# Kernel optimization log

Hardware: AMD Instinct MI355X
Metric: run time of the kernel (lower is better)

## Reference

```python
import jax, jax.numpy as jnp
import numpy as np

HID = 4096; H = 128; P = 64; N = 128; G = 8; K = 4; CH = 128
INTER = H * P                      # 8192
CONV_DIM = INTER + 2 * G * N       # 10240
PROJ = INTER + CONV_DIM + H        # 18560
EPS = 1e-5


def segsum(x):
    # stable segment-sum: out[..., i, j] = sum_{j < k <= i} x[..., k]; -inf above diagonal
    T = x.shape[-1]
    xe = jnp.repeat(x[..., None], T, axis=-1)          # [..., i, j] = x[..., i]
    strict = jnp.tril(jnp.ones((T, T), bool), -1)
    s = jnp.cumsum(jnp.where(strict, xe, 0.0), axis=-2)
    keep = jnp.tril(jnp.ones((T, T), bool), 0)
    return jnp.where(keep, s, -jnp.inf)


def setup_inputs() -> dict:
    key = jax.random.key(0)
    ks = jax.random.split(key, 6)
    b, L = 2, 2048
    hidden_states = jax.random.normal(ks[0], (b, L, HID), jnp.float32)
    in_proj_w = jax.random.normal(ks[1], (PROJ, HID), jnp.float32) * (HID ** -0.5)
    conv_w = jax.random.normal(ks[2], (CONV_DIM, 1, K), jnp.float32) * 0.2
    conv_b = jax.random.normal(ks[3], (CONV_DIM,), jnp.float32) * 0.02
    dt_bias = jnp.ones((H,), jnp.float32)
    A_log = jnp.log(jnp.arange(1, H + 1, dtype=jnp.float32))
    D = jnp.ones((H,), jnp.float32)
    norm_weight = jnp.ones((INTER,), jnp.float32)
    out_proj_w = jax.random.normal(ks[4], (HID, INTER), jnp.float32) * (INTER ** -0.5)
    return dict(hidden_states=hidden_states, in_proj_w=in_proj_w, conv_w=conv_w, conv_b=conv_b,
                dt_bias=dt_bias, A_log=A_log, D=D, norm_weight=norm_weight, out_proj_w=out_proj_w)


def _mamba2(hidden_states, in_proj_w, conv_w, conv_b, dt_bias, A_log, D, norm_weight, out_proj_w):
    b, L, _ = hidden_states.shape
    nchunk = L // CH  # seq_len chosen to be a multiple of chunk_size (pad_size = 0)

    # in_proj and split into gate | conv path (x,B,C) | dt
    proj = hidden_states @ in_proj_w.T
    gate, hBC, dt = jnp.split(proj, [INTER, INTER + CONV_DIM], axis=-1)

    # causal depthwise conv1d (padding k-1, truncate) + SiLU
    xp = jnp.pad(hBC.transpose(0, 2, 1), ((0, 0), (0, 0), (K - 1, 0)))
    xc = jax.lax.conv_general_dilated(xp, conv_w, (1,), 'VALID',
                                      feature_group_count=CONV_DIM,
                                      dimension_numbers=('NCW', 'OIW', 'NCW'))
    hBC = jax.nn.silu((xc + conv_b[None, :, None]).transpose(0, 2, 1))
    hs, Bx, Cx = jnp.split(hBC, [INTER, INTER + G * N], axis=-1)

    A = -jnp.exp(A_log)                      # [H]
    dt = jax.nn.softplus(dt + dt_bias)       # time_step_limit = (0, inf) -> clamp is no-op

    hs = hs.reshape(b, L, H, P)
    rep = H // G
    Bm = jnp.tile(Bx.reshape(b, L, G, N), (1, 1, rep, 1))   # matches torch .repeat
    Cm = jnp.tile(Cx.reshape(b, L, G, N), (1, 1, rep, 1))

    D_res = D[None, None, :, None] * hs      # [b,L,H,P]

    # discretize and chunk
    X = (hs * dt[..., None]).reshape(b, nchunk, CH, H, P)
    A_dt = (A[None, None, :] * dt).reshape(b, nchunk, CH, H).transpose(0, 3, 1, 2)  # [b,H,c,l]
    Bc = Bm.reshape(b, nchunk, CH, H, N)
    Cc = Cm.reshape(b, nchunk, CH, H, N)
    A_cs = jnp.cumsum(A_dt, axis=-1)

    # 1. intra-chunk (diagonal blocks)
    Lmat = jnp.exp(segsum(A_dt))                              # [b,H,c,l,s]
    Gm = jnp.einsum('bclhn,bcshn->bclsh', Cc, Bc)
    M = Gm * Lmat.transpose(0, 2, 3, 4, 1)                    # [b,c,l,s,H]
    Y_diag = jnp.einsum('bclsh,bcshp->bclhp', M, X)

    # 2. per-chunk states
    decay_states = jnp.exp(A_cs[..., -1:] - A_cs)             # [b,H,c,l]
    B_decay = Bc * decay_states.transpose(0, 2, 3, 1)[..., None]
    states = jnp.einsum('bclhn,bclhp->bchpn', B_decay, X)     # [b,c,H,P,N]

    # 3. inter-chunk recurrence
    states = jnp.concatenate([jnp.zeros_like(states[:, :1]), states], axis=1)
    A_last = jnp.pad(A_cs[..., -1], ((0, 0), (0, 0), (1, 0)))  # [b,H,c+1]
    decay_chunk = jnp.exp(segsum(A_last)).transpose(0, 3, 2, 1)  # [b,c+1,c+1,H]
    new_states = jnp.einsum('bzjh,bzhpn->bjhpn', decay_chunk, states)
    prev_states = new_states[:, :-1]                           # [b,c,H,P,N]

    # 4. state -> output
    sdo = jnp.exp(A_cs).transpose(0, 2, 3, 1)                  # [b,c,l,H]
    Y_off = jnp.einsum('bclhn,bchpn->bclhp', Cc, prev_states) * sdo[..., None]

    y = (Y_diag + Y_off).reshape(b, L, H, P) + D_res
    scan_out = y.reshape(b, L, INTER)

    # gated group RMSNorm (norm_before_gate=False: gate first, then group-RMS)
    xg = scan_out * jax.nn.silu(gate)
    xr = xg.reshape(b, L, G, INTER // G)
    xr = xr * jax.lax.rsqrt(jnp.mean(xr * xr, axis=-1, keepdims=True) + EPS)
    normed = xr.reshape(b, L, INTER) * norm_weight

    return normed @ out_proj_w.T


def reference(hidden_states, in_proj_w, conv_w, conv_b, dt_bias, A_log, D, norm_weight, out_proj_w):
    return _mamba2(hidden_states, in_proj_w, conv_w, conv_b, dt_bias, A_log, D, norm_weight, out_proj_w)
```

## Files before the change

kernel.cpp:

```cpp
#include <hip/hip_runtime.h>

#define NH 128
#define PD 64
#define NSD 128
#define NG 8
#define CHK 128
#define HIDD 4096
#define INTER_D 8192
#define CONV_D 10240
#define PROJ_D 18560
#define SEQ 2048
#define ROWS 4096
#define NCH 16

typedef __attribute__((ext_vector_type(8))) short bf16x8;
typedef __attribute__((ext_vector_type(4))) float f32x4;

__device__ __forceinline__ unsigned short f2bf(float f) {
  unsigned int u = __float_as_uint(f);
  u += 0x7FFF + ((u >> 16) & 1);
  return (unsigned short)(u >> 16);
}
__device__ __forceinline__ float bf2f(unsigned short s) {
  return __uint_as_float(((unsigned int)s) << 16);
}

__device__ __forceinline__ void gld16(const unsigned short* g, unsigned short* l) {
  __builtin_amdgcn_global_load_lds(
      (__attribute__((address_space(1))) const void*)g,
      (__attribute__((address_space(3))) void*)l, 16, 0, 0);
}

#define BAR() __builtin_amdgcn_s_barrier()
#define SCHED() __builtin_amdgcn_sched_barrier(0)
#define VMCNT(n) asm volatile("s_waitcnt vmcnt(" #n ")" ::: "memory")

__device__ __forceinline__ bf16x8 ldsfrag(const unsigned short* slot, int row, int kslot) {
  int byte = row * 128 + (((kslot ^ (row & 7)) << 4));
  return *(const bf16x8*)((const char*)slot + byte);
}

__global__ __launch_bounds__(256) void cvt_kernel(const float* __restrict__ in,
                                                  unsigned short* __restrict__ out,
                                                  size_t n) {
  size_t i = ((size_t)blockIdx.x * 256 + threadIdx.x) * 4;
  if (i < n) {
    float4 f = *(const float4*)(in + i);
    ushort4 o;
    o.x = f2bf(f.x); o.y = f2bf(f.y); o.z = f2bf(f.z); o.w = f2bf(f.w);
    *(ushort4*)(out + i) = o;
  }
}

template <int OUT_BF16>
__global__ __launch_bounds__(512, 2) void gemm256(const unsigned short* __restrict__ A,
                                                  const unsigned short* __restrict__ B,
                                                  unsigned short* __restrict__ outb,
                                                  float* __restrict__ outf,
                                                  int Nreal, int Ks, int Kl, int koff) {
  __shared__ unsigned short lds[8][8192];
  int tid = threadIdx.x, l = tid & 63, w = tid >> 6;
  int wm = w >> 2, wn = w & 3;
  int il = l & 15, fog = l >> 4;
  int bid = blockIdx.x;
  int xcd = bid & 7, local = bid >> 3;
  int mt = xcd * 2 + (local & 1), nt = local >> 1;
  const unsigned short* Abase = A + (size_t)mt * 256 * Ks + koff;
  const unsigned short* Bbase = B + (size_t)nt * 256 * Ks + koff;
  int NT = Kl >> 6;

  f32x4 acc[2][2][4][2];
#pragma unroll
  for (int a = 0; a < 2; ++a)
#pragma unroll
    for (int b = 0; b < 2; ++b)
#pragma unroll
      for (int m = 0; m < 4; ++m)
#pragma unroll
        for (int n = 0; n < 2; ++n) acc[a][b][m][n] = (f32x4){0.f, 0.f, 0.f, 0.f};

  auto STG = [&](int tt, int ty) {
    int tc = tt < NT ? tt : NT - 1;
    const unsigned short* g = ((ty & 1) ? Bbase : Abase) + (size_t)((ty >> 1) * 128) * Ks + tc * 64;
    unsigned short* sp = (unsigned short*)lds[(tt & 1) * 4 + ty];
#pragma unroll
    for (int j = 0; j < 2; ++j) {
      int row = (j * 8 + w) * 8 + (l >> 3);
      int scol = ((l & 7) ^ (row & 7)) * 8;
      gld16(g + (size_t)row * Ks + scol, sp + (j * 8 + w) * 512);
    }
  };

#define LDA(SLOT)                                          \
  _Pragma("unroll") for (int mi = 0; mi < 4; ++mi)         \
  _Pragma("unroll") for (int kk = 0; kk < 2; ++kk)         \
      av[mi][kk] = ldsfrag(SLOT, wm * 64 + mi * 16 + il, kk * 4 + fog);
#define LDB(QN, SLOT)                                      \
  _Pragma("unroll") for (int ni = 0; ni < 2; ++ni)         \
  _Pragma("unroll") for (int kk = 0; kk < 2; ++kk)         \
      bv[QN][ni][kk] = ldsfrag(SLOT, wn * 32 + ni * 16 + il, kk * 4 + fog);
#define MFMA_PH(QM, QN)                                    \
  _Pragma("unroll") for (int mi = 0; mi < 4; ++mi)         \
  _Pragma("unroll") for (int ni = 0; ni < 2; ++ni)         \
  _Pragma("unroll") for (int kk = 0; kk < 2; ++kk)         \
      acc[QM][QN][mi][ni] = __builtin_amdgcn_mfma_f32_16x16x32_bf16( \
          av[mi][kk], bv[QN][ni][kk], acc[QM][QN][mi][ni], 0, 0, 0);

  STG(0, 0); STG(0, 1); STG(0, 3); STG(0, 2);
  VMCNT(2);
  BAR(); SCHED();

  for (int t = 0; t < NT; ++t) {
    const unsigned short* sA0 = lds[(t & 1) * 4 + 0];
    const unsigned short* sB0 = lds[(t & 1) * 4 + 1];
    const unsigned short* sA1 = lds[(t & 1) * 4 + 2];
    const unsigned short* sB1 = lds[(t & 1) * 4 + 3];
    bf16x8 av[4][2], bv[2][2][2];
    LDA(sA0); LDB(0, sB0); LDB(1, sB1);
    STG(t + 1, 0); STG(t + 1, 1);
    BAR();
    __builtin_amdgcn_s_setprio(1);
    MFMA_PH(0, 0);
    __builtin_amdgcn_s_setprio(0);
    VMCNT(4);
    BAR(); SCHED();
    STG(t + 1, 3);
    __builtin_amdgcn_s_setprio(1);
    MFMA_PH(0, 1);
    __builtin_amdgcn_s_setprio(0);
    BAR();
    LDA(sA1);
    STG(t + 1, 2);
    BAR();
    __builtin_amdgcn_s_setprio(1);
    MFMA_PH(1, 0);
    __builtin_amdgcn_s_setprio(0);
    BAR();
    __builtin_amdgcn_s_setprio(1);
    MFMA_PH(1, 1);
    __builtin_amdgcn_s_setprio(0);
    VMCNT(2);
    BAR(); SCHED();
  }
  VMCNT(0);

  int rl = (l >> 4) * 4;
#pragma unroll
  for (int qm = 0; qm < 2; ++qm)
#pragma unroll
    for (int qn = 0; qn < 2; ++qn)
#pragma unroll
      for (int mi = 0; mi < 4; ++mi)
#pragma unroll
        for (int ni = 0; ni < 2; ++ni) {
          int grow = mt * 256 + qm * 128 + wm * 64 + mi * 16 + rl;
          int gcol = nt * 256 + qn * 128 + wn * 32 + ni * 16 + il;
          if (!OUT_BF16 || gcol < Nreal) {
#pragma unroll
            for (int r = 0; r < 4; ++r) {
              float v = acc[qm][qn][mi][ni][r];
              if (OUT_BF16)
                outb[(size_t)(grow + r) * Nreal + gcol] = f2bf(v);
              else
                outf[(size_t)(grow + r) * Nreal + gcol] = v;
            }
          }
        }
#undef LDA
#undef LDB
#undef MFMA_PH
}

__global__ __launch_bounds__(128) void dts_kernel(const unsigned short* __restrict__ proj,
                                                  const float* __restrict__ dt_bias,
                                                  const float* __restrict__ A_log,
                                                  float* __restrict__ dtg,
                                                  float* __restrict__ acsg) {
  int bc = blockIdx.x;
  int h = threadIdx.x;
  int b = bc >> 4, c = bc & 15;
  float A = -__expf(A_log[h]);
  float bias = dt_bias[h];
  float cum = 0.f;
  int row0 = b * SEQ + c * CHK;
#pragma unroll 4
  for (int ll = 0; ll < CHK; ++ll) {
    float x = bf2f(proj[(size_t)(row0 + ll) * PROJ_D + (PROJ_D - NH) + h]) + bias;
    float d = (x > 20.f) ? x : log1pf(expf(x));
    dtg[(size_t)(row0 + ll) * NH + h] = d;
    cum += A * d;
    acsg[(((size_t)bc * NH) + h) * CHK + ll] = cum;
  }
}

__global__ __launch_bounds__(256) void conv_kernel(const unsigned short* __restrict__ proj,
                                                   const float* __restrict__ cw,
                                                   const float* __restrict__ cb,
                                                   unsigned short* __restrict__ xbc) {
  int ch0 = (blockIdx.x * 256 + threadIdx.x) * 8;
  int row = blockIdx.y;
  int b = row >> 11, ll = row & 2047;
  float4 cwv[8];
#pragma unroll
  for (int e = 0; e < 8; ++e) cwv[e] = *(const float4*)(cw + (ch0 + e) * 4);
  float acc[8];
#pragma unroll
  for (int e = 0; e < 8; ++e) acc[e] = cb[ch0 + e];
#pragma unroll
  for (int k = 0; k < 4; ++k) {
    int l2 = ll - 3 + k;
    if (l2 >= 0) {
      bf16x8 v = *(const bf16x8*)(proj + (size_t)(b * SEQ + l2) * PROJ_D + INTER_D + ch0);
#pragma unroll
      for (int e = 0; e < 8; ++e)
        acc[e] += bf2f(((unsigned short*)&v)[e]) * ((const float*)&cwv[e])[k];
    }
  }
  unsigned short o[8];
#pragma unroll
  for (int e = 0; e < 8; ++e) {
    float s = acc[e] / (1.f + __expf(-acc[e]));
    o[e] = f2bf(s);
  }
  *(int4*)(xbc + (size_t)row * CONV_D + ch0) = *(int4*)o;
}

__global__ __launch_bounds__(256) void e1b_kernel(const unsigned short* __restrict__ xbc,
                                                  const float* __restrict__ dtg,
                                                  const float* __restrict__ acsg,
                                                  unsigned short* __restrict__ states16) {
  int bid = blockIdx.x;
  int h = bid & 127, c = (bid >> 7) & 15, b = bid >> 11;
  int g = h & 7;
  int row0 = b * SEQ + c * CHK;
  __shared__ __align__(16) char smem[52736];
  unsigned short* XT = (unsigned short*)smem;
  unsigned short* BdT = (unsigned short*)(smem + 17408);
  float* Acs = (float*)(smem + 52224);
  int tid = threadIdx.x, lane = tid & 63, wv = tid >> 6;
  int fo = (lane >> 4) * 8, il = lane & 15, rl = (lane >> 4) * 4;
  if (tid < 128) Acs[tid] = acsg[(((size_t)(b * NCH + c) * NH) + h) * CHK + tid];
  __syncthreads();
#pragma unroll
  for (int j = 0; j < 4; ++j) {
    int q = tid + j * 256;
    int ll = q >> 3, p0 = (q & 7) * 8;
    int row = row0 + ll;
    float dtv = dtg[(size_t)row * NH + h];
    int4 raw = *(const int4*)(xbc + (size_t)row * CONV_D + h * PD + p0);
    unsigned short* u = (unsigned short*)&raw;
#pragma unroll
    for (int e = 0; e < 8; ++e) XT[(p0 + e) * 136 + ll] = f2bf(bf2f(u[e]) * dtv);
  }
#pragma unroll
  for (int j = 0; j < 8; ++j) {
    int q = tid + j * 256;
    int ll = q >> 4, n0 = (q & 15) * 8;
    float dec = __expf(Acs[CHK - 1] - Acs[ll]);
    int4 raw = *(const int4*)(xbc + (size_t)(row0 + ll) * CONV_D + INTER_D + g * NSD + n0);
    unsigned short* u = (unsigned short*)&raw;
#pragma unroll
    for (int e = 0; e < 8; ++e) BdT[(n0 + e) * 136 + ll] = f2bf(bf2f(u[e]) * dec);
  }
  __syncthreads();
  f32x4 st[8];
#pragma unroll
  for (int i = 0; i < 8; ++i) st[i] = (f32x4){0.f, 0.f, 0.f, 0.f};
#pragma unroll
  for (int ks = 0; ks < 4; ++ks) {
    bf16x8 a = *(const bf16x8*)&XT[(wv * 16 + il) * 136 + ks * 32 + fo];
#pragma unroll
    for (int ni = 0; ni < 8; ++ni) {
      bf16x8 bb = *(const bf16x8*)&BdT[(ni * 16 + il) * 136 + ks * 32 + fo];
      st[ni] = __builtin_amdgcn_mfma_f32_16x16x32_bf16(a, bb, st[ni], 0, 0, 0);
    }
  }
  size_t base = ((size_t)(b * NH + h) * NCH + c) * (PD * NSD);
#pragma unroll
  for (int ni = 0; ni < 8; ++ni) {
    int n = ni * 16 + il;
#pragma unroll
    for (int r = 0; r < 4; ++r) {
      int p = wv * 16 + rl + r;
      states16[base + p * NSD + n] = f2bf(st[ni][r]);
    }
  }
}

__global__ __launch_bounds__(256) void e2_kernel(const float* __restrict__ acsg,
                                                 const unsigned short* __restrict__ states16,
                                                 unsigned short* __restrict__ prevs) {
  int bid = blockIdx.x;
  int bh = bid >> 2, pg = bid & 3;
  int b = bh >> 7;
  int t = threadIdx.x;
  float S[8];
#pragma unroll
  for (int j = 0; j < 8; ++j) S[j] = 0.f;
  for (int c = 0; c < NCH; ++c) {
    float alast = acsg[(((size_t)((b * NCH + c) * NH) + (bh & 127))) * CHK + (CHK - 1)];
    float dec = __expf(alast);
    size_t base = ((size_t)bh * NCH + c) * (PD * NSD) + (size_t)pg * 2048 + (size_t)t * 8;
    bf16x8 v = *(const bf16x8*)(states16 + base);
    unsigned short o[8];
#pragma unroll
    for (int j = 0; j < 8; ++j) {
      o[j] = f2bf(S[j]);
      S[j] = S[j] * dec + bf2f(((unsigned short*)&v)[j]);
    }
    *(bf16x8*)(prevs + base) = *(bf16x8*)o;
  }
}

__global__ __launch_bounds__(512) void e13_kernel(const unsigned short* __restrict__ xbc,
                                                  const float* __restrict__ dtg,
                                                  const float* __restrict__ acsg,
                                                  const unsigned short* __restrict__ prevs,
                                                  const float* __restrict__ Dp,
                                                  unsigned short* __restrict__ ybh) {
  int bid = blockIdx.x;
  int h = bid & 127, c = (bid >> 7) & 15, b = bid >> 11;
  int g = h & 7;
  int row0 = b * SEQ + c * CHK;
  __shared__ __align__(16) char smem[70144];
  unsigned short* Cst = (unsigned short*)smem;
  unsigned short* Bst = (unsigned short*)(smem + 10240);
  unsigned short* Mt = (unsigned short*)smem;
  unsigned short* XT = (unsigned short*)(smem + 34816);
  unsigned short* Sp = (unsigned short*)(smem + 52224);
  float* Acs = (float*)(smem + 69632);
  int tid = threadIdx.x, lane = tid & 63, wv = tid >> 6;
  int fo = (lane >> 4) * 8, il = lane & 15, rl = (lane >> 4) * 4;
  if (tid < 128) Acs[tid] = acsg[(((size_t)(b * NCH + c) * NH) + h) * CHK + tid];

  f32x4 gm[8];
#pragma unroll
  for (int i = 0; i < 8; ++i) gm[i] = (f32x4){0.f, 0.f, 0.f, 0.f};
  bf16x8 cf[4];
  int srow = tid >> 2, scol = (tid & 3) * 8;
#pragma unroll
  for (int kc = 0; kc < 4; ++kc) {
    __syncthreads();
    *(int4*)(Cst + srow * 40 + scol) =
        *(const int4*)(xbc + (size_t)(row0 + srow) * CONV_D + INTER_D + NG * NSD + g * NSD + kc * 32 + scol);
    *(int4*)(Bst + srow * 40 + scol) =
        *(const int4*)(xbc + (size_t)(row0 + srow) * CONV_D + INTER_D + g * NSD + kc * 32 + scol);
    __syncthreads();
    bf16x8 a = *(const bf16x8*)&Cst[(wv * 16 + il) * 40 + fo];
    cf[kc] = a;
#pragma unroll
    for (int ni = 0; ni < 8; ++ni) {
      bf16x8 bb = *(const bf16x8*)&Bst[(ni * 16 + il) * 40 + fo];
      gm[ni] = __builtin_amdgcn_mfma_f32_16x16x32_bf16(a, bb, gm[ni], 0, 0, 0);
    }
  }
  __syncthreads();
#pragma unroll
  for (int ni = 0; ni < 8; ++ni) {
    int s = ni * 16 + il;
#pragma unroll
    for (int r = 0; r < 4; ++r) {
      int ll = wv * 16 + rl + r;
      float v = (s <= ll) ? gm[ni][r] * __expf(Acs[ll] - Acs[s]) : 0.f;
      Mt[ll * 136 + s] = f2bf(v);
    }
  }
#pragma unroll
  for (int j = 0; j < 2; ++j) {
    int q = tid + j * 512;
    int ll = q >> 3, p0 = (q & 7) * 8;
    int row = row0 + ll;
    float dtv = dtg[(size_t)row * NH + h];
    int4 raw = *(const int4*)(xbc + (size_t)row * CONV_D + h * PD + p0);
    unsigned short* u = (unsigned short*)&raw;
#pragma unroll
    for (int e = 0; e < 8; ++e) XT[(p0 + e) * 136 + ll] = f2bf(bf2f(u[e]) * dtv);
  }
  size_t sbase = ((size_t)(b * NH + h) * NCH + c) * (PD * NSD);
#pragma unroll
  for (int j = 0; j < 2; ++j) {
    int q = tid + j * 512;
    int p = q >> 4, n0 = (q & 15) * 8;
    *(int4*)(Sp + p * 136 + n0) = *(const int4*)(prevs + sbase + p * NSD + n0);
  }
  __syncthreads();
  f32x4 yd[4], yo[4];
#pragma unroll
  for (int i = 0; i < 4; ++i) {
    yd[i] = (f32x4){0.f, 0.f, 0.f, 0.f};
    yo[i] = (f32x4){0.f, 0.f, 0.f, 0.f};
  }
#pragma unroll
  for (int ks = 0; ks < 4; ++ks) {
    bf16x8 a = *(const bf16x8*)&Mt[(wv * 16 + il) * 136 + ks * 32 + fo];
#pragma unroll
    for (int pi = 0; pi < 4; ++pi) {
      bf16x8 bb = *(const bf16x8*)&XT[(pi * 16 + il) * 136 + ks * 32 + fo];
      bf16x8 sb = *(const bf16x8*)&Sp[(pi * 16 + il) * 136 + ks * 32 + fo];
      yd[pi] = __builtin_amdgcn_mfma_f32_16x16x32_bf16(a, bb, yd[pi], 0, 0, 0);
      yo[pi] = __builtin_amdgcn_mfma_f32_16x16x32_bf16(cf[ks], sb, yo[pi], 0, 0, 0);
    }
  }
  float dv = Dp[h];
#pragma unroll
  for (int pi = 0; pi < 4; ++pi) {
    int p = pi * 16 + il;
#pragma unroll
    for (int r = 0; r < 4; ++r) {
      int ll = wv * 16 + rl + r;
      int row = row0 + ll;
      float hsv = bf2f(xbc[(size_t)row * CONV_D + h * PD + p]);
      ybh[(size_t)row * INTER_D + h * PD + p] =
          f2bf(yd[pi][r] + yo[pi][r] * __expf(Acs[ll]) + dv * hsv);
    }
  }
}

__global__ __launch_bounds__(256) void fnorm_kernel(const unsigned short* __restrict__ ybh,
                                                    const unsigned short* __restrict__ proj,
                                                    const float* __restrict__ nw,
                                                    unsigned short* __restrict__ normed) {
  int row = blockIdx.x >> 3;
  int gg = blockIdx.x & 7;
  int t = threadIdx.x;
  int ch = gg * 1024 + t * 4;
  ushort4 yv = *(const ushort4*)(ybh + (size_t)row * INTER_D + ch);
  ushort4 gv = *(const ushort4*)(proj + (size_t)row * PROJ_D + ch);
  float v[4];
  float ss = 0.f;
  {
    const unsigned short* yp = (const unsigned short*)&yv;
    const unsigned short* gp = (const unsigned short*)&gv;
#pragma unroll
    for (int j = 0; j < 4; ++j) {
      float val = bf2f(yp[j]);
      float gt = bf2f(gp[j]);
      val *= gt / (1.f + __expf(-gt));
      v[j] = val;
      ss += val * val;
    }
  }
#pragma unroll
  for (int o = 1; o < 64; o <<= 1) ss += __shfl_xor(ss, o, 64);
  __shared__ float sred[4];
  if ((t & 63) == 0) sred[t >> 6] = ss;
  __syncthreads();
  float tot = sred[0] + sred[1] + sred[2] + sred[3];
  float rms = rsqrtf(tot / 1024.f + 1e-5f);
  float4 nwv = *(const float4*)(nw + ch);
  unsigned short o4[4];
  const float* nwp = (const float*)&nwv;
#pragma unroll
  for (int j = 0; j < 4; ++j) o4[j] = f2bf(v[j] * rms * nwp[j]);
  *(ushort4*)(normed + (size_t)row * INTER_D + ch) = *(ushort4*)o4;
}

extern "C" void kernel_launch(void* const* d_in, const int* in_sizes, int n_in,
                              void* d_out, int out_size, void* d_ws, size_t ws_size,
                              hipStream_t stream) {
  (void)in_sizes; (void)n_in; (void)out_size; (void)ws_size;
  const float* hs = (const float*)d_in[0];
  const float* w1 = (const float*)d_in[1];
  const float* cw = (const float*)d_in[2];
  const float* cb = (const float*)d_in[3];
  const float* dtb = (const float*)d_in[4];
  const float* alog = (const float*)d_in[5];
  const float* Dp = (const float*)d_in[6];
  const float* nw = (const float*)d_in[7];
  const float* w2 = (const float*)d_in[8];
  float* out = (float*)d_out;
  char* ws = (char*)d_ws;

  unsigned short* hsb = (unsigned short*)(ws);
  unsigned short* w1b = (unsigned short*)(ws + 33554432);
  unsigned short* w2b = (unsigned short*)(ws + 186646528);
  unsigned short* proj = (unsigned short*)(ws + 253755392);
  unsigned short* xbc = (unsigned short*)(ws + 405798912);
  float* dtg = (float*)(ws + 489684992);
  float* acsg = (float*)(ws + 491782144);
  unsigned short* states16 = (unsigned short*)(ws + 493879296);
  unsigned short* prevs = (unsigned short*)(ws + 560988160);
  unsigned short* ybh = (unsigned short*)(ws + 628097024);
  unsigned short* normed = (unsigned short*)(ws);

  cvt_kernel<<<dim3(16384), dim3(256), 0, stream>>>(hs, hsb, (size_t)ROWS * HIDD);
  cvt_kernel<<<dim3(74240), dim3(256), 0, stream>>>(w1, w1b, (size_t)PROJ_D * HIDD);
  cvt_kernel<<<dim3(32768), dim3(256), 0, stream>>>(w2, w2b, (size_t)HIDD * INTER_D);

  gemm256<1><<<dim3(16 * 73), dim3(512), 0, stream>>>(hsb, w1b, proj, nullptr,
                                                      PROJ_D, HIDD, HIDD, 0);
  dts_kernel<<<dim3(32), dim3(128), 0, stream>>>(proj, dtb, alog, dtg, acsg);
  conv_kernel<<<dim3(5, 4096), dim3(256), 0, stream>>>(proj, cw, cb, xbc);
  e1b_kernel<<<dim3(4096), dim3(256), 0, stream>>>(xbc, dtg, acsg, states16);
  e2_kernel<<<dim3(1024), dim3(256), 0, stream>>>(acsg, states16, prevs);
  e13_kernel<<<dim3(4096), dim3(512), 0, stream>>>(xbc, dtg, acsg, prevs, Dp, ybh);
  fnorm_kernel<<<dim3(32768), dim3(256), 0, stream>>>(ybh, proj, nw, normed);
  gemm256<0><<<dim3(16 * 16), dim3(512), 0, stream>>>(normed, w2b, nullptr, out,
                                                      HIDD, INTER_D, INTER_D, 0);
}
```

Measured before the change: 1.376 ms.

## Merge conversion launches, split dt scan into parallel pass, widen norm

New measurement: 1.313 ms. 1.05x faster.

```diff
diff --git a/kernel.cpp b/kernel.cpp
--- a/kernel.cpp
+++ b/kernel.cpp
@@ -40,16 +40,28 @@
   return *(const bf16x8*)((const char*)slot + byte);
 }
 
-__global__ __launch_bounds__(256) void cvt_kernel(const float* __restrict__ in,
-                                                  unsigned short* __restrict__ out,
-                                                  size_t n) {
-  size_t i = ((size_t)blockIdx.x * 256 + threadIdx.x) * 4;
-  if (i < n) {
-    float4 f = *(const float4*)(in + i);
-    ushort4 o;
-    o.x = f2bf(f.x); o.y = f2bf(f.y); o.z = f2bf(f.z); o.w = f2bf(f.w);
-    *(ushort4*)(out + i) = o;
-  }
+__global__ __launch_bounds__(256) void cvt_all_kernel(const float* __restrict__ hs,
+                                                      const float* __restrict__ w1,
+                                                      const float* __restrict__ w2,
+                                                      unsigned short* __restrict__ hsb,
+                                                      unsigned short* __restrict__ w1b,
+                                                      unsigned short* __restrict__ w2b) {
+  int bid = blockIdx.x;
+  const float* in;
+  unsigned short* out;
+  size_t base;
+  if (bid < 16384) {
+    in = hs; out = hsb; base = (size_t)bid * 1024;
+  } else if (bid < 16384 + 74240) {
+    in = w1; out = w1b; base = (size_t)(bid - 16384) * 1024;
+  } else {
+    in = w2; out = w2b; base = (size_t)(bid - 16384 - 74240) * 1024;
+  }
+  size_t i = base + (size_t)threadIdx.x * 4;
+  float4 f = *(const float4*)(in + i);
+  ushort4 o;
+  o.x = f2bf(f.x); o.y = f2bf(f.y); o.z = f2bf(f.z); o.w = f2bf(f.w);
+  *(ushort4*)(out + i) = o;
 }
 
 template <int OUT_BF16>
@@ -171,24 +183,28 @@
 #undef MFMA_PH
 }
 
-__global__ __launch_bounds__(128) void dts_kernel(const unsigned short* __restrict__ proj,
-                                                  const float* __restrict__ dt_bias,
-                                                  const float* __restrict__ A_log,
-                                                  float* __restrict__ dtg,
-                                                  float* __restrict__ acsg) {
+__global__ __launch_bounds__(256) void dtsa_kernel(const unsigned short* __restrict__ proj,
+                                                   const float* __restrict__ dt_bias,
+                                                   float* __restrict__ dtg) {
+  int idx = blockIdx.x * 256 + threadIdx.x;
+  int row = idx >> 7, h = idx & 127;
+  float x = bf2f(proj[(size_t)row * PROJ_D + (PROJ_D - NH) + h]) + dt_bias[h];
+  float d = (x > 20.f) ? x : log1pf(expf(x));
+  dtg[(size_t)row * NH + h] = d;
+}
+
+__global__ __launch_bounds__(128) void dtsb_kernel(const float* __restrict__ dtg,
+                                                   const float* __restrict__ A_log,
+                                                   float* __restrict__ acsg) {
   int bc = blockIdx.x;
   int h = threadIdx.x;
   int b = bc >> 4, c = bc & 15;
   float A = -__expf(A_log[h]);
-  float bias = dt_bias[h];
   float cum = 0.f;
   int row0 = b * SEQ + c * CHK;
-#pragma unroll 4
+#pragma unroll 8
   for (int ll = 0; ll < CHK; ++ll) {
-    float x = bf2f(proj[(size_t)(row0 + ll) * PROJ_D + (PROJ_D - NH) + h]) + bias;
-    float d = (x > 20.f) ? x : log1pf(expf(x));
-    dtg[(size_t)(row0 + ll) * NH + h] = d;
-    cum += A * d;
+    cum += A * dtg[(size_t)(row0 + ll) * NH + h];
     acsg[(((size_t)bc * NH) + h) * CHK + ll] = cum;
   }
 }
@@ -420,39 +436,43 @@
                                                     const unsigned short* __restrict__ proj,
                                                     const float* __restrict__ nw,
                                                     unsigned short* __restrict__ normed) {
-  int row = blockIdx.x >> 3;
-  int gg = blockIdx.x & 7;
-  int t = threadIdx.x;
-  int ch = gg * 1024 + t * 4;
-  ushort4 yv = *(const ushort4*)(ybh + (size_t)row * INTER_D + ch);
-  ushort4 gv = *(const ushort4*)(proj + (size_t)row * PROJ_D + ch);
-  float v[4];
+  int gid = blockIdx.x * 4 + (threadIdx.x >> 6);
+  int lane = threadIdx.x & 63;
+  int row = gid >> 3, gg = gid & 7;
+  int ch = gg * 1024 + lane * 16;
+  bf16x8 y0 = *(const bf16x8*)(ybh + (size_t)row * INTER_D + ch);
+  bf16x8 y1 = *(const bf16x8*)(ybh + (size_t)row * INTER_D + ch + 8);
+  bf16x8 g0 = *(const bf16x8*)(proj + (size_t)row * PROJ_D + ch);
+  bf16x8 g1 = *(const bf16x8*)(proj + (size_t)row * PROJ_D + ch + 8);
+  float v[16];
   float ss = 0.f;
-  {
-    const unsigned short* yp = (const unsigned short*)&yv;
-    const unsigned short* gp = (const unsigned short*)&gv;
-#pragma unroll
-    for (int j = 0; j < 4; ++j) {
-      float val = bf2f(yp[j]);
-      float gt = bf2f(gp[j]);
-      val *= gt / (1.f + __expf(-gt));
-      v[j] = val;
-      ss += val * val;
-    }
+#pragma unroll
+  for (int j = 0; j < 8; ++j) {
+    float val = bf2f(((unsigned short*)&y0)[j]);
+    float gt = bf2f(((unsigned short*)&g0)[j]);
+    val *= gt / (1.f + __expf(-gt));
+    v[j] = val; ss += val * val;
+  }
+#pragma unroll
+  for (int j = 0; j < 8; ++j) {
+    float val = bf2f(((unsigned short*)&y1)[j]);
+    float gt = bf2f(((unsigned short*)&g1)[j]);
+    val *= gt / (1.f + __expf(-gt));
+    v[8 + j] = val; ss += val * val;
   }
 #pragma unroll
   for (int o = 1; o < 64; o <<= 1) ss += __shfl_xor(ss, o, 64);
-  __shared__ float sred[4];
-  if ((t & 63) == 0) sred[t >> 6] = ss;
-  __syncthreads();
-  float tot = sred[0] + sred[1] + sred[2] + sred[3];
-  float rms = rsqrtf(tot / 1024.f + 1e-5f);
-  float4 nwv = *(const float4*)(nw + ch);
-  unsigned short o4[4];
-  const float* nwp = (const float*)&nwv;
-#pragma unroll
-  for (int j = 0; j < 4; ++j) o4[j] = f2bf(v[j] * rms * nwp[j]);
-  *(ushort4*)(normed + (size_t)row * INTER_D + ch) = *(ushort4*)o4;
+  float rms = rsqrtf(ss / 1024.f + 1e-5f);
+  unsigned short o16[16];
+#pragma unroll
+  for (int q = 0; q < 4; ++q) {
+    float4 nwv = *(const float4*)(nw + ch + q * 4);
+    const float* nwp = (const float*)&nwv;
+#pragma unroll
+    for (int j = 0; j < 4; ++j) o16[q * 4 + j] = f2bf(v[q * 4 + j] * rms * nwp[j]);
+  }
+  *(int4*)(normed + (size_t)row * INTER_D + ch) = *(int4*)o16;
+  *(int4*)(normed + (size_t)row * INTER_D + ch + 8) = *(int4*)(o16 + 8);
 }
 
 extern "C" void kernel_launch(void* const* d_in, const int* in_sizes, int n_in,
@@ -483,18 +503,17 @@
   unsigned short* ybh = (unsigned short*)(ws + 628097024);
   unsigned short* normed = (unsigned short*)(ws);
 
-  cvt_kernel<<<dim3(16384), dim3(256), 0, stream>>>(hs, hsb, (size_t)ROWS * HIDD);
-  cvt_kernel<<<dim3(74240), dim3(256), 0, stream>>>(w1, w1b, (size_t)PROJ_D * HIDD);
-  cvt_kernel<<<dim3(32768), dim3(256), 0, stream>>>(w2, w2b, (size_t)HIDD * INTER_D);
+  cvt_all_kernel<<<dim3(123392), dim3(256), 0, stream>>>(hs, w1, w2, hsb, w1b, w2b);
 
   gemm256<1><<<dim3(16 * 73), dim3(512), 0, stream>>>(hsb, w1b, proj, nullptr,
                                                       PROJ_D, HIDD, HIDD, 0);
-  dts_kernel<<<dim3(32), dim3(128), 0, stream>>>(proj, dtb, alog, dtg, acsg);
+  dtsa_kernel<<<dim3(2048), dim3(256), 0, stream>>>(proj, dtb, dtg);
+  dtsb_kernel<<<dim3(32), dim3(128), 0, stream>>>(dtg, alog, acsg);
   conv_kernel<<<dim3(5, 4096), dim3(256), 0, stream>>>(proj, cw, cb, xbc);
   e1b_kernel<<<dim3(4096), dim3(256), 0, stream>>>(xbc, dtg, acsg, states16);
   e2_kernel<<<dim3(1024), dim3(256), 0, stream>>>(acsg, states16, prevs);
   e13_kernel<<<dim3(4096), dim3(512), 0, stream>>>(xbc, dtg, acsg, prevs, Dp, ybh);
-  fnorm_kernel<<<dim3(32768), dim3(256), 0, stream>>>(ybh, proj, nw, normed);
+  fnorm_kernel<<<dim3(8192), dim3(256), 0, stream>>>(ybh, proj, nw, normed);
   gemm256<0><<<dim3(16 * 16), dim3(512), 0, stream>>>(normed, w2b, nullptr, out,
                                                       HIDD, INTER_D, INTER_D, 0);
 }
```
